# Optimization experiments

Measured on AMD Instinct MI355X. Metric: run time of the kernel, lower is better.

## Reference

```python
import jax, jax.numpy as jnp
import numpy as np

B = 16384      # batch
CNUM = 2048    # codebook entries
K = 8          # topk
D = 10         # emb_dim
M = 50         # meta_dim
UID = 1000000
IID = 1000000
TAU = 10.0


def setup_inputs() -> dict:
    key = jax.random.key(0)
    ks = jax.random.split(key, 14)
    uid_col = jax.random.randint(ks[0], (B, 1), 0, UID, dtype=jnp.int64)
    iid_col = jax.random.randint(ks[1], (B, 1), 0, IID + 1, dtype=jnp.int64)
    x = jnp.concatenate([uid_col, iid_col], axis=1)
    return {
        "x": x,
        "gumbel_u_src": jax.random.uniform(ks[2], (B, CNUM), dtype=jnp.float32),
        "gumbel_u_tgt": jax.random.uniform(ks[3], (B, CNUM), dtype=jnp.float32),
        "src_uid_table": jax.random.normal(ks[4], (UID, D), dtype=jnp.float32),
        "tgt_uid_table": jax.random.normal(ks[5], (UID, D), dtype=jnp.float32),
        "tgt_iid_table": jax.random.normal(ks[6], (IID + 1, D), dtype=jnp.float32),
        "C": jax.random.normal(ks[7], (CNUM, M), dtype=jnp.float32) * 0.01,
        "w1": jax.random.normal(ks[8], (D, M), dtype=jnp.float32) * 0.01,
        "w2": jax.random.normal(ks[9], (M, D), dtype=jnp.float32) * 0.01,
        "mw1": jax.random.normal(ks[10], (D + M, 50), dtype=jnp.float32) * 0.1,
        "mb1": jnp.zeros((50,), dtype=jnp.float32),
        "mw2": jax.random.normal(ks[11], (50, D * D), dtype=jnp.float32) * 0.1,
        "mb2": jnp.zeros((D * D,), dtype=jnp.float32),
    }


def _gumbel_route(u_emb, C, w1, u_noise):
    # u_emb: [B, D] -> logits s_u: [B, CNUM]
    s = jnp.einsum('bm,cm->bc', u_emb @ w1, C)
    g = -jnp.log(-jnp.log(u_noise + 1e-20) + 1e-20)  # gumbel noise
    gw = jax.nn.softmax((s + g) / TAU, axis=-1)       # F.gumbel_softmax, hard=False
    tw, ti = jax.lax.top_k(gw, K)                     # [B, K]
    c_u = C[ti]                                       # [B, K, M] codebook gather
    return tw, ti, c_u


def reference(x, gumbel_u_src, gumbel_u_tgt, src_uid_table, tgt_uid_table,
              tgt_iid_table, C, w1, w2, mw1, mb1, mw2, mb2):
    # ---- stage == 'test_meta' ----
    # target-side interest embedding ('test_interst' path)
    tuid = tgt_uid_table[x[:, 0]]                      # [B, D]
    tw_t, _, c_t = _gumbel_route(tuid, C, w1, gumbel_u_tgt)
    tuid_ins = ((c_t * tw_t[..., None]).sum(axis=1)) @ w2   # [B, D]
    # source-side routing ('test_meta' path of InterstEmbedding)
    uid = src_uid_table[x[:, 0]]                       # [B, D]
    tw_s, _, c_s = _gumbel_route(uid, C, w1, gumbel_u_src)
    src_fea = jnp.broadcast_to(uid[:, None, :], (uid.shape[0], K, D))  # [B, K, D]
    inp = jnp.concatenate([c_s, src_fea], axis=-1)     # [B, K, M+D] = [B, K, 60]
    h = jax.nn.relu(inp @ mw1 + mb1)                   # [B, K, 50]
    mapping = (h @ mw2 + mb2).reshape(-1, K, D, D)     # per-sample hypernet weights
    src_emb = jnp.einsum('bkd,bkde->bke', src_fea, mapping)  # [B, K, D]
    pre_emb = (src_emb * tw_s[..., None]).sum(axis=1)  # [B, D]
    fin_emb = tuid_ins + pre_emb                       # [B, D]
    iid_emb = tgt_iid_table[x[:, 1]]                   # [B, D]
    return jnp.sum(fin_emb * iid_emb, axis=-1)         # [B]
```

## Files before the change

kernel.cpp:

```cpp
#include <hip/hip_runtime.h>
#include <hip/hip_bf16.h>


#define BROWS 16384
#define CNUM  2048
#define KSEL  8
#define DIMD  10
#define MDIM  50
#define RPB   16
#define RTPB  32
#define TAUI  0.1f
#define T24   24

#define OFF_PF   0
#define OFF_T24  1664
#define OFF_T24L 2432
#define OFF_TS   3200
#define OFF_TW   8832
#define OFF_TI   9088
#define OFF_UD   9344
#define SMEM_W   9536

typedef float    f32x4 __attribute__((ext_vector_type(4)));
typedef _Float16 half8 __attribute__((ext_vector_type(8)));
typedef float    flt2  __attribute__((ext_vector_type(2)));
typedef unsigned int u32;

__device__ __forceinline__ u32 pkrtz(float a, float b) {
    auto h = __builtin_amdgcn_cvt_pkrtz(a, b);
    union { decltype(h) v; u32 u; } c; c.v = h; return c.u;
}
__device__ __forceinline__ float gnoise(float u) {
    return -__logf(-__logf(u + 1e-20f) + 1e-20f);
}

__global__ void cvtC(const float* __restrict__ Cm, u32* __restrict__ C16) {
    const int j = blockIdx.x * 256 + threadIdx.x;
    const int cand = j >> 5, w = j & 31, k = 2 * w;
    const float a = (k < MDIM)     ? Cm[cand*MDIM + k]     : 0.f;
    const float b = (k + 1 < MDIM) ? Cm[cand*MDIM + k + 1] : 0.f;
    C16[j] = pkrtz(a, b);
}

template<bool PRE>
__global__ __launch_bounds__(256, 4)
void mf_fused(const int* __restrict__ x32,
              const float* __restrict__ gsrc,
              const float* __restrict__ gtgt,
              const float* __restrict__ suid,
              const float* __restrict__ tuid,
              const float* __restrict__ tiid,
              const float* __restrict__ Cm,
              const float* __restrict__ w1,
              const float* __restrict__ w2,
              const float* __restrict__ mw1,
              const float* __restrict__ mb1,
              const float* __restrict__ mw2,
              const float* __restrict__ mb2,
              const u32* __restrict__ C16,
              float* __restrict__ out)
{
    __shared__ __align__(16) float smem[SMEM_W];
    __shared__ int sFlag;
    float* sPf  = smem + OFF_PF;
    u32*   T24u = (u32*)(smem + OFF_T24);
    float* T24l = smem + OFF_T24L;

    const int tid  = threadIdx.x;
    const int row0 = blockIdx.x * RPB;

    if (tid == 0) sFlag = 1;
    __syncthreads();
    if (tid < 128) { if (x32[2*tid+1] != 0) atomicAnd(&sFlag, 0); }
    __syncthreads();
    const int is64 = sFlag;

    for (int t = tid; t < RTPB*52; t += 256) {
        const int rt = t / 52, mm = t - rt*52;
        float v = 0.f;
        if (mm < MDIM) {
            const int r = row0 + (rt >> 1);
            const int uidx = is64 ? x32[4*r] : x32[2*r];
            const float* tab = (rt & 1) ? suid : tuid;
            #pragma unroll
            for (int d = 0; d < DIMD; ++d) v += tab[uidx*DIMD + d] * w1[d*MDIM + mm];
        }
        sPf[t] = v;
    }
    __syncthreads();

    const int lane = tid & 63, wv = tid >> 6;
    const int lr = lane & 15, lk = lane >> 4;
    const int g = wv & 1, h = wv >> 1;
    const int rt = g*16 + lr;
    const float* up = ((lr & 1) ? gsrc : gtgt) + (size_t)(row0 + g*8 + (lr >> 1)) * CNUM;

    half8 b0, b1;
    {
        union { u32 u[4]; half8 v; } c0, c1;
        #pragma unroll
        for (int jj = 0; jj < 4; ++jj) {
            const int k0 = lk*8 + jj*2;
            c0.u[jj] = pkrtz(sPf[rt*52 + k0], sPf[rt*52 + k0 + 1]);
            const int k1 = 32 + lk*8 + jj*2;
            const float e0 = (k1     < 52) ? sPf[rt*52 + k1]     : 0.f;
            const float e1 = (k1 + 1 < 52) ? sPf[rt*52 + k1 + 1] : 0.f;
            c1.u[jj] = pkrtz(e0, e1);
        }
        b0 = c0.v; b1 = c1.v;
    }

    float ts = 0.f;
    float q0=-3.4e38f,q1=-3.4e38f,q2=-3.4e38f,q3=-3.4e38f,
          q4=-3.4e38f,q5=-3.4e38f,q6=-3.4e38f,q7=-3.4e38f;

    #pragma unroll 4
    for (int ti = 0; ti < 64; ++ti) {
        const int cb = ((ti >> 2) << 7) + h*64 + ((ti & 3) << 4);
        half8 a0, a1;
        if (PRE) {
            const u32* cr = C16 + (size_t)(cb + lr)*32 + lk*4;
            a0 = *(const half8*)cr;
            a1 = *(const half8*)(cr + 16);
        } else {
            const float* cr = Cm + (size_t)(cb + lr)*MDIM;
            union { u32 u[4]; half8 v; } c0, c1;
            #pragma unroll
            for (int jj = 0; jj < 4; ++jj) {
                const int k0 = lk*8 + jj*2;
                c0.u[jj] = pkrtz(cr[k0], cr[k0+1]);
                const int k1 = 32 + lk*8 + jj*2;
                const float e0 = (k1     < MDIM) ? cr[k1]     : 0.f;
                const float e1 = (k1 + 1 < MDIM) ? cr[k1+1] : 0.f;
                c1.u[jj] = pkrtz(e0, e1);
            }
            a0 = c0.v; a1 = c1.v;
        }
        f32x4 acc = {0.f, 0.f, 0.f, 0.f};
        acc = __builtin_amdgcn_mfma_f32_16x16x32_f16(a0, b0, acc, 0, 0, 0);
        acc = __builtin_amdgcn_mfma_f32_16x16x32_f16(a1, b1, acc, 0, 0, 0);
        const f32x4 u4 = *(const f32x4*)(up + cb + lk*4);
        const int cg = cb + lk*4;
        #pragma unroll
        for (int r4 = 0; r4 < 4; ++r4) {
            const float l = (acc[r4] + gnoise(u4[r4])) * TAUI;
            ts += __expf(l);
            const float xs = __uint_as_float(
                (__float_as_uint(l) & 0xFFFFF800u) | (u32)(cg + r4));
            q0 = fmaxf(q0, fminf(q1, xs));
            q1 = fmaxf(q1, fminf(q2, xs));
            q2 = fmaxf(q2, fminf(q3, xs));
            q3 = fmaxf(q3, fminf(q4, xs));
            q4 = fmaxf(q4, fminf(q5, xs));
            q5 = fmaxf(q5, fminf(q6, xs));
            q6 = fmaxf(q6, fminf(q7, xs));
            q7 = fmaxf(q7, xs);
        }
    }

    {
        float tss = ts;
        tss += __shfl_xor(tss, 16); tss += __shfl_xor(tss, 32);
        if (lk == 0) smem[OFF_TS + rt*2 + h] = tss;
        #pragma unroll
        for (int k = 0; k < 12; ++k) {
            float gm = fmaxf(q7, __shfl_xor(q7, 16));
            gm = fmaxf(gm, __shfl_xor(gm, 32));
            if (q7 == gm) {
                T24u[rt*T24 + h*12 + k] = __float_as_uint(q7);
                q7=q6; q6=q5; q5=q4; q4=q3; q3=q2; q2=q1; q1=q0; q0=-3.4e38f;
            }
        }
    }
    __syncthreads();

    for (int e = tid; e < RTPB*T24; e += 256) {
        const int ert = e / T24;
        const int idx = (int)(T24u[e] & 2047u);
        const float* pf = sPf + ert*52;
        const float* cr = Cm + idx*MDIM;
        float s = 0.f;
        #pragma unroll
        for (int k2 = 0; k2 < 25; ++k2) {
            flt2 c = *(const flt2*)(cr + k2*2);
            s += pf[2*k2] * c.x + pf[2*k2+1] * c.y;
        }
        const int r = row0 + (ert >> 1);
        const float u = ((ert & 1) ? gsrc : gtgt)[(size_t)r*CNUM + idx];
        T24l[e] = (s + gnoise(u)) * TAUI;
    }
    __syncthreads();

    if (tid < RTPB) {
        const int rrt = tid;
        const float inv = 1.0f / (smem[OFF_TS + rrt*2] + smem[OFF_TS + rrt*2 + 1]);
        float lv[T24]; int iv[T24];
        #pragma unroll
        for (int j = 0; j < T24; ++j) {
            lv[j] = T24l[rrt*T24 + j];
            iv[j] = (int)(T24u[rrt*T24 + j] & 2047u);
        }
        u32 used = 0;
        #pragma unroll
        for (int k = 0; k < KSEL; ++k) {
            float bl = -3.4e38f; int bi = 1 << 30; int bj = 0;
            #pragma unroll
            for (int j = 0; j < T24; ++j) {
                const bool ok = !((used >> j) & 1);
                if (ok && (lv[j] > bl || (lv[j] == bl && iv[j] < bi))) { bl = lv[j]; bi = iv[j]; bj = j; }
            }
            used |= 1u << bj;
            smem[OFF_TW + rrt*KSEL + k] = __expf(bl) * inv;
            ((int*)smem)[OFF_TI + rrt*KSEL + k] = bi;
        }
    }
    __syncthreads();

    float* sH    = smem;
    float* sQ    = smem + 832;
    float* sUd   = smem + OFF_UD;
    float* sTopW = smem + OFF_TW;
    int*   sTopI = (int*)smem + OFF_TI;

    const int gg = tid >> 4, lg = tid & 15;
    const int row = row0 + gg;
    const int rt_t = gg*2, rt_s = gg*2 + 1;
    const int uidx = is64 ? x32[4*row]     : x32[2*row];
    const int iidx = is64 ? x32[4*row + 2] : x32[2*row + 1];

    if (lg < DIMD) sUd[gg*12 + lg] = suid[uidx*DIMD + lg];
    __syncthreads();

    for (int t = lg; t < MDIM*DIMD; t += 16) {
        const int j = t / DIMD, e = t - j*DIMD;
        float q = 0.f;
        #pragma unroll
        for (int d = 0; d < DIMD; ++d) q += sUd[gg*12 + d] * mw2[j*(DIMD*DIMD) + d*DIMD + e];
        sQ[gg*500 + t] = q;
    }
    for (int mm = lg; mm < MDIM; mm += 16) {
        float v = 0.f;
        #pragma unroll
        for (int k = 0; k < KSEL; ++k)
            v += sTopW[rt_t*KSEL + k] * Cm[sTopI[rt_t*KSEL + k]*MDIM + mm];
        sH[gg*52 + mm] = v;
    }
    __syncthreads();

    float acc_e = 0.f, be = 0.f;
    if (lg < DIMD) {
        for (int m2 = 0; m2 < MDIM; ++m2) acc_e += sH[gg*52 + m2] * w2[m2*DIMD + lg];
        #pragma unroll
        for (int d = 0; d < DIMD; ++d) be += sUd[gg*12 + d] * mb2[d*DIMD + lg];
    }
    __syncthreads();

    for (int k = 0; k < KSEL; ++k) {
        const int   ik = sTopI[rt_s*KSEL + k];
        const float tw = sTopW[rt_s*KSEL + k];
        for (int j = lg; j < MDIM; j += 16) {
            float hh = mb1[j];
            const float* crow = Cm + ik*MDIM;
            for (int t2 = 0; t2 < MDIM; ++t2) hh += crow[t2] * mw1[t2*MDIM + j];
            #pragma unroll
            for (int d = 0; d < DIMD; ++d) hh += sUd[gg*12 + d] * mw1[(MDIM + d)*MDIM + j];
            sH[gg*52 + j] = fmaxf(hh, 0.f);
        }
        __syncthreads();
        if (lg < DIMD) {
            float se = be;
            for (int j = 0; j < MDIM; ++j) se += sH[gg*52 + j] * sQ[gg*500 + j*DIMD + lg];
            acc_e += tw * se;
        }
        __syncthreads();
    }

    float o = 0.f;
    if (lg < DIMD) o = acc_e * tiid[iidx*DIMD + lg];
    #pragma unroll
    for (int k = 8; k >= 1; k >>= 1) o += __shfl_xor(o, k, 16);
    if (lg == 0) out[row] = o;
}

extern "C" void kernel_launch(void* const* d_in, const int* in_sizes, int n_in,
                              void* d_out, int out_size, void* d_ws, size_t ws_size,
                              hipStream_t stream) {
    (void)in_sizes; (void)n_in; (void)out_size;
    const int*   x32  = (const int*)d_in[0];
    const float* gsrc = (const float*)d_in[1];
    const float* gtgt = (const float*)d_in[2];
    const float* suid = (const float*)d_in[3];
    const float* tuid = (const float*)d_in[4];
    const float* tiid = (const float*)d_in[5];
    const float* Cm   = (const float*)d_in[6];
    const float* w1   = (const float*)d_in[7];
    const float* w2   = (const float*)d_in[8];
    const float* mw1  = (const float*)d_in[9];
    const float* mb1  = (const float*)d_in[10];
    const float* mw2  = (const float*)d_in[11];
    const float* mb2  = (const float*)d_in[12];
    u32* C16 = (u32*)d_ws;

    if (ws_size >= 262144) {
        hipLaunchKernelGGL(cvtC, dim3(256), dim3(256), 0, stream, Cm, C16);
        hipLaunchKernelGGL(mf_fused<true>, dim3(BROWS/RPB), dim3(256), 0, stream,
                           x32, gsrc, gtgt, suid, tuid, tiid, Cm, w1, w2, mw1, mb1, mw2, mb2,
                           C16, (float*)d_out);
    } else {
        hipLaunchKernelGGL(mf_fused<false>, dim3(BROWS/RPB), dim3(256), 0, stream,
                           x32, gsrc, gtgt, suid, tuid, tiid, Cm, w1, w2, mw1, mb1, mw2, mb2,
                           C16, (float*)d_out);
    }
}
```

Baseline: 282.5 us.

## Pre-swizzle fp16 codebook into MFMA fragment layout and software-prefetch loads

The codebook conversion kernel now writes fp16 C in a per-lane MFMA fragment order, so each lane reads contiguous 16-byte chunks with coalesced wave-wide loads. The main loop in the precomputed path becomes a software pipeline: the gumbel noise tiles are prefetched four iterations ahead and the codebook fragments two iterations ahead in registers. This targets load latency and uncoalesced access in the routing loop. It doubles the workspace requirement (the larger layout stores padding) and raises register pressure, which could lower occupancy; if the workspace is smaller, the slower fallback path runs.

```diff
diff --git a/kernel.cpp b/kernel.cpp
--- a/kernel.cpp
+++ b/kernel.cpp
@@ -36,7 +36,10 @@
 
 __global__ void cvtC(const float* __restrict__ Cm, u32* __restrict__ C16) {
     const int j = blockIdx.x * 256 + threadIdx.x;
-    const int cand = j >> 5, w = j & 31, k = 2 * w;
+    const int w = j & 3, l = (j >> 2) & 63, pl = (j >> 8) & 1, Tg = j >> 9;
+    const int cand = Tg * 16 + (l & 15);
+    const int kk = pl * 16 + ((l >> 4) << 2) + w;
+    const int k = 2 * kk;
     const float a = (k < MDIM)     ? Cm[cand*MDIM + k]     : 0.f;
     const float b = (k + 1 < MDIM) ? Cm[cand*MDIM + k + 1] : 0.f;
     C16[j] = pkrtz(a, b);
@@ -114,33 +117,7 @@
     float q0=-3.4e38f,q1=-3.4e38f,q2=-3.4e38f,q3=-3.4e38f,
           q4=-3.4e38f,q5=-3.4e38f,q6=-3.4e38f,q7=-3.4e38f;
 
-    #pragma unroll 4
-    for (int ti = 0; ti < 64; ++ti) {
-        const int cb = ((ti >> 2) << 7) + h*64 + ((ti & 3) << 4);
-        half8 a0, a1;
-        if (PRE) {
-            const u32* cr = C16 + (size_t)(cb + lr)*32 + lk*4;
-            a0 = *(const half8*)cr;
-            a1 = *(const half8*)(cr + 16);
-        } else {
-            const float* cr = Cm + (size_t)(cb + lr)*MDIM;
-            union { u32 u[4]; half8 v; } c0, c1;
-            #pragma unroll
-            for (int jj = 0; jj < 4; ++jj) {
-                const int k0 = lk*8 + jj*2;
-                c0.u[jj] = pkrtz(cr[k0], cr[k0+1]);
-                const int k1 = 32 + lk*8 + jj*2;
-                const float e0 = (k1     < MDIM) ? cr[k1]     : 0.f;
-                const float e1 = (k1 + 1 < MDIM) ? cr[k1+1] : 0.f;
-                c1.u[jj] = pkrtz(e0, e1);
-            }
-            a0 = c0.v; a1 = c1.v;
-        }
-        f32x4 acc = {0.f, 0.f, 0.f, 0.f};
-        acc = __builtin_amdgcn_mfma_f32_16x16x32_f16(a0, b0, acc, 0, 0, 0);
-        acc = __builtin_amdgcn_mfma_f32_16x16x32_f16(a1, b1, acc, 0, 0, 0);
-        const f32x4 u4 = *(const f32x4*)(up + cb + lk*4);
-        const int cg = cb + lk*4;
+    auto select4 = [&](const f32x4& acc, const f32x4& u4, int cg) {
         #pragma unroll
         for (int r4 = 0; r4 < 4; ++r4) {
             const float l = (acc[r4] + gnoise(u4[r4])) * TAUI;
@@ -155,6 +132,82 @@
             q5 = fmaxf(q5, fminf(q6, xs));
             q6 = fmaxf(q6, fminf(q7, xs));
             q7 = fmaxf(q7, xs);
+        }
+    };
+
+    if (PRE) {
+        auto uaddr = [&](int t) -> const float* {
+            return up + (((t >> 2) << 7) + h*64 + ((t & 3) << 4) + lk*4);
+        };
+        auto caddr = [&](int t) -> const u32* {
+            const int Tg = ((t >> 2) << 3) + (h << 2) + (t & 3);
+            return C16 + ((size_t)(Tg * 2) * 64 + lane) * 4;
+        };
+        f32x4 ub0 = *(const f32x4*)uaddr(0);
+        f32x4 ub1 = *(const f32x4*)uaddr(1);
+        f32x4 ub2 = *(const f32x4*)uaddr(2);
+        f32x4 ub3 = *(const f32x4*)uaddr(3);
+        const u32* ca0 = caddr(0);
+        const u32* ca1 = caddr(1);
+        half8 a00 = *(const half8*)ca0;
+        half8 a10 = *(const half8*)(ca0 + 256);
+        half8 a01 = *(const half8*)ca1;
+        half8 a11 = *(const half8*)(ca1 + 256);
+
+        for (int tt = 0; tt < 64; tt += 4) {
+            #pragma unroll
+            for (int p = 0; p < 4; ++p) {
+                const int t = tt + p;
+                f32x4 u4;
+                if      (p == 0) u4 = ub0;
+                else if (p == 1) u4 = ub1;
+                else if (p == 2) u4 = ub2;
+                else             u4 = ub3;
+                half8 a0, a1;
+                if ((p & 1) == 0) { a0 = a00; a1 = a10; }
+                else              { a0 = a01; a1 = a11; }
+                {
+                    const int tu = (t + 4) & 63;
+                    const f32x4 un = *(const f32x4*)uaddr(tu);
+                    if      (p == 0) ub0 = un;
+                    else if (p == 1) ub1 = un;
+                    else if (p == 2) ub2 = un;
+                    else             ub3 = un;
+                }
+                {
+                    const int tc = (t + 2) & 63;
+                    const u32* ca = caddr(tc);
+                    const half8 an0 = *(const half8*)ca;
+                    const half8 an1 = *(const half8*)(ca + 256);
+                    if ((p & 1) == 0) { a00 = an0; a10 = an1; }
+                    else              { a01 = an0; a11 = an1; }
+                }
+                const int cb = ((t >> 2) << 7) + h*64 + ((t & 3) << 4);
+                f32x4 acc = {0.f, 0.f, 0.f, 0.f};
+                acc = __builtin_amdgcn_mfma_f32_16x16x32_f16(a0, b0, acc, 0, 0, 0);
+                acc = __builtin_amdgcn_mfma_f32_16x16x32_f16(a1, b1, acc, 0, 0, 0);
+                select4(acc, u4, cb + lk*4);
+            }
+        }
+    } else {
+        for (int t = 0; t < 64; ++t) {
+            const int cb = ((t >> 2) << 7) + h*64 + ((t & 3) << 4);
+            const float* cr = Cm + (size_t)(cb + lr)*MDIM;
+            union { u32 u[4]; half8 v; } c0, c1;
+            #pragma unroll
+            for (int jj = 0; jj < 4; ++jj) {
+                const int k0 = lk*8 + jj*2;
+                c0.u[jj] = pkrtz(cr[k0], cr[k0+1]);
+                const int k1 = 32 + lk*8 + jj*2;
+                const float e0 = (k1     < MDIM) ? cr[k1]   : 0.f;
+                const float e1 = (k1 + 1 < MDIM) ? cr[k1+1] : 0.f;
+                c1.u[jj] = pkrtz(e0, e1);
+            }
+            f32x4 acc = {0.f, 0.f, 0.f, 0.f};
+            acc = __builtin_amdgcn_mfma_f32_16x16x32_f16(c0.v, b0, acc, 0, 0, 0);
+            acc = __builtin_amdgcn_mfma_f32_16x16x32_f16(c1.v, b1, acc, 0, 0, 0);
+            const f32x4 u4 = *(const f32x4*)(up + cb + lk*4);
+            select4(acc, u4, cb + lk*4);
         }
     }
 
@@ -301,8 +354,8 @@
     const float* mb2  = (const float*)d_in[12];
     u32* C16 = (u32*)d_ws;
 
-    if (ws_size >= 262144) {
-        hipLaunchKernelGGL(cvtC, dim3(256), dim3(256), 0, stream, Cm, C16);
+    if (ws_size >= 524288) {
+        hipLaunchKernelGGL(cvtC, dim3(512), dim3(256), 0, stream, Cm, C16);
         hipLaunchKernelGGL(mf_fused<true>, dim3(BROWS/RPB), dim3(256), 0, stream,
                            x32, gsrc, gtgt, suid, tuid, tiid, Cm, w1, w2, mw1, mb1, mw2, mb2,
                            C16, (float*)d_out);
```

Result: faster. 266.8 us (-5.6%).

## Split fused kernel into routing and epilogue kernels with MFMA-ordered codebook layout

Applied to the files above, without the earlier changes.

Splits the single fused kernel into a routing kernel and a separate epilogue kernel, which exchange top-k weights and indices through workspace memory. The routing kernel now handles 8 batch rows per block, with each wave covering a contiguous quarter of the codebook, and launch bounds rise to 8 blocks per SM for more occupancy. The codebook is pre-packed into fp16 in MFMA fragment order so each lane's loads are coalesced. The epilogue algebraically folds the item embedding into the hypernet weights per thread, avoiding shared-memory staging. This costs an extra launch plus a global round trip for the top-k results, and needs a larger workspace, falling back to the old fused path if the workspace is too small.

```diff
diff --git a/kernel.cpp b/kernel.cpp
--- a/kernel.cpp
+++ b/kernel.cpp
@@ -7,24 +7,13 @@
 #define KSEL  8
 #define DIMD  10
 #define MDIM  50
-#define RPB   16
-#define RTPB  32
 #define TAUI  0.1f
-#define T24   24
-
-#define OFF_PF   0
-#define OFF_T24  1664
-#define OFF_T24L 2432
-#define OFF_TS   3200
-#define OFF_TW   8832
-#define OFF_TI   9088
-#define OFF_UD   9344
-#define SMEM_W   9536
 
 typedef float    f32x4 __attribute__((ext_vector_type(4)));
 typedef _Float16 half8 __attribute__((ext_vector_type(8)));
 typedef float    flt2  __attribute__((ext_vector_type(2)));
 typedef unsigned int u32;
+typedef unsigned long long u64;
 
 __device__ __forceinline__ u32 pkrtz(float a, float b) {
     auto h = __builtin_amdgcn_cvt_pkrtz(a, b);
@@ -36,38 +25,36 @@
 
 __global__ void cvtC(const float* __restrict__ Cm, u32* __restrict__ C16) {
     const int j = blockIdx.x * 256 + threadIdx.x;
-    const int cand = j >> 5, w = j & 31, k = 2 * w;
+    const int w = j & 3, l = (j >> 2) & 63, pl = (j >> 8) & 1, Tg = j >> 9;
+    const int cand = Tg * 16 + (l & 15);
+    const int kk = pl * 16 + ((l >> 4) << 2) + w;
+    const int k = 2 * kk;
     const float a = (k < MDIM)     ? Cm[cand*MDIM + k]     : 0.f;
     const float b = (k + 1 < MDIM) ? Cm[cand*MDIM + k + 1] : 0.f;
     C16[j] = pkrtz(a, b);
 }
 
-template<bool PRE>
-__global__ __launch_bounds__(256, 4)
-void mf_fused(const int* __restrict__ x32,
+__global__ __launch_bounds__(256, 8)
+void mf_route(const int* __restrict__ x32,
               const float* __restrict__ gsrc,
               const float* __restrict__ gtgt,
               const float* __restrict__ suid,
               const float* __restrict__ tuid,
-              const float* __restrict__ tiid,
               const float* __restrict__ Cm,
               const float* __restrict__ w1,
-              const float* __restrict__ w2,
-              const float* __restrict__ mw1,
-              const float* __restrict__ mb1,
-              const float* __restrict__ mw2,
-              const float* __restrict__ mb2,
               const u32* __restrict__ C16,
-              float* __restrict__ out)
+              float* __restrict__ gTW,
+              int*   __restrict__ gTI)
 {
-    __shared__ __align__(16) float smem[SMEM_W];
+    __shared__ __align__(16) float smem[2432];
     __shared__ int sFlag;
-    float* sPf  = smem + OFF_PF;
-    u32*   T24u = (u32*)(smem + OFF_T24);
-    float* T24l = smem + OFF_T24L;
+    float* sPf  = smem;
+    u32*   T48u = (u32*)(smem + 832);
+    float* T48l = smem + 1600;
+    float* TS   = smem + 2368;
 
     const int tid  = threadIdx.x;
-    const int row0 = blockIdx.x * RPB;
+    const int row0 = blockIdx.x * 8;
 
     if (tid == 0) sFlag = 1;
     __syncthreads();
@@ -75,7 +62,7 @@
     __syncthreads();
     const int is64 = sFlag;
 
-    for (int t = tid; t < RTPB*52; t += 256) {
+    for (int t = tid; t < 16*52; t += 256) {
         const int rt = t / 52, mm = t - rt*52;
         float v = 0.f;
         if (mm < MDIM) {
@@ -91,9 +78,8 @@
 
     const int lane = tid & 63, wv = tid >> 6;
     const int lr = lane & 15, lk = lane >> 4;
-    const int g = wv & 1, h = wv >> 1;
-    const int rt = g*16 + lr;
-    const float* up = ((lr & 1) ? gsrc : gtgt) + (size_t)(row0 + g*8 + (lr >> 1)) * CNUM;
+    const int rt = lr;
+    const float* up = ((lr & 1) ? gsrc : gtgt) + (size_t)(row0 + (lr >> 1)) * CNUM;
 
     half8 b0, b1;
     {
@@ -114,32 +100,15 @@
     float q0=-3.4e38f,q1=-3.4e38f,q2=-3.4e38f,q3=-3.4e38f,
           q4=-3.4e38f,q5=-3.4e38f,q6=-3.4e38f,q7=-3.4e38f;
 
-    #pragma unroll 4
-    for (int ti = 0; ti < 64; ++ti) {
-        const int cb = ((ti >> 2) << 7) + h*64 + ((ti & 3) << 4);
-        half8 a0, a1;
-        if (PRE) {
-            const u32* cr = C16 + (size_t)(cb + lr)*32 + lk*4;
-            a0 = *(const half8*)cr;
-            a1 = *(const half8*)(cr + 16);
-        } else {
-            const float* cr = Cm + (size_t)(cb + lr)*MDIM;
-            union { u32 u[4]; half8 v; } c0, c1;
-            #pragma unroll
-            for (int jj = 0; jj < 4; ++jj) {
-                const int k0 = lk*8 + jj*2;
-                c0.u[jj] = pkrtz(cr[k0], cr[k0+1]);
-                const int k1 = 32 + lk*8 + jj*2;
-                const float e0 = (k1     < MDIM) ? cr[k1]     : 0.f;
-                const float e1 = (k1 + 1 < MDIM) ? cr[k1+1] : 0.f;
-                c1.u[jj] = pkrtz(e0, e1);
-            }
-            a0 = c0.v; a1 = c1.v;
-        }
+    for (int t = 0; t < 32; ++t) {
+        const int cb = wv*512 + t*16;
+        const f32x4 u4 = *(const f32x4*)(up + cb + lk*4);
+        const u32* cp = C16 + (size_t)((wv*32 + t)*128 + lane)*4;
+        const half8 a0 = *(const half8*)cp;
+        const half8 a1 = *(const half8*)(cp + 256);
         f32x4 acc = {0.f, 0.f, 0.f, 0.f};
         acc = __builtin_amdgcn_mfma_f32_16x16x32_f16(a0, b0, acc, 0, 0, 0);
         acc = __builtin_amdgcn_mfma_f32_16x16x32_f16(a1, b1, acc, 0, 0, 0);
-        const f32x4 u4 = *(const f32x4*)(up + cb + lk*4);
         const int cg = cb + lk*4;
         #pragma unroll
         for (int r4 = 0; r4 < 4; ++r4) {
@@ -161,21 +130,316 @@
     {
         float tss = ts;
         tss += __shfl_xor(tss, 16); tss += __shfl_xor(tss, 32);
-        if (lk == 0) smem[OFF_TS + rt*2 + h] = tss;
+        if (lk == 0) TS[rt*4 + wv] = tss;
         #pragma unroll
         for (int k = 0; k < 12; ++k) {
             float gm = fmaxf(q7, __shfl_xor(q7, 16));
             gm = fmaxf(gm, __shfl_xor(gm, 32));
             if (q7 == gm) {
-                T24u[rt*T24 + h*12 + k] = __float_as_uint(q7);
+                T48u[rt*48 + wv*12 + k] = __float_as_uint(q7);
                 q7=q6; q6=q5; q5=q4; q4=q3; q3=q2; q2=q1; q1=q0; q0=-3.4e38f;
             }
         }
     }
     __syncthreads();
 
-    for (int e = tid; e < RTPB*T24; e += 256) {
-        const int ert = e / T24;
+    for (int e = tid; e < 16*48; e += 256) {
+        const int ert = e / 48;
+        const int idx = (int)(T48u[e] & 2047u);
+        const float* pf = sPf + ert*52;
+        const float* cr = Cm + idx*MDIM;
+        float s = 0.f;
+        #pragma unroll
+        for (int k2 = 0; k2 < 25; ++k2) {
+            flt2 c = *(const flt2*)(cr + k2*2);
+            s += pf[2*k2] * c.x + pf[2*k2+1] * c.y;
+        }
+        const int r = row0 + (ert >> 1);
+        const float u = ((ert & 1) ? gsrc : gtgt)[(size_t)r*CNUM + idx];
+        T48l[e] = (s + gnoise(u)) * TAUI;
+    }
+    __syncthreads();
+
+    if (tid < 16) {
+        const int r8 = tid;
+        const float inv = 1.0f / (TS[r8*4] + TS[r8*4+1] + TS[r8*4+2] + TS[r8*4+3]);
+        u64 used = 0;
+        for (int k = 0; k < KSEL; ++k) {
+            float bl = -3.4e38f; int bi = 1 << 30; int bj = 0;
+            for (int j = 0; j < 48; ++j) {
+                if ((used >> j) & 1ull) continue;
+                const float lv = T48l[r8*48 + j];
+                const int   iv = (int)(T48u[r8*48 + j] & 2047u);
+                if (lv > bl || (lv == bl && iv < bi)) { bl = lv; bi = iv; bj = j; }
+            }
+            used |= 1ull << bj;
+            const int grt = blockIdx.x*16 + r8;
+            gTW[grt*KSEL + k] = __expf(bl) * inv;
+            gTI[grt*KSEL + k] = bi;
+        }
+    }
+}
+
+__global__ __launch_bounds__(256, 4)
+void mf_epilog(const int* __restrict__ x32,
+               const float* __restrict__ suid,
+               const float* __restrict__ tiid,
+               const float* __restrict__ Cm,
+               const float* __restrict__ w2,
+               const float* __restrict__ mw1,
+               const float* __restrict__ mb1,
+               const float* __restrict__ mw2,
+               const float* __restrict__ mb2,
+               const float* __restrict__ gTW,
+               const int*   __restrict__ gTI,
+               float* __restrict__ out)
+{
+    __shared__ int sFlag;
+    const int tid = threadIdx.x;
+    const int g = tid >> 4, lg = tid & 15;
+    const int row = blockIdx.x * 16 + g;
+
+    if (tid == 0) sFlag = 1;
+    __syncthreads();
+    if (tid < 128) { if (x32[2*tid+1] != 0) atomicAnd(&sFlag, 0); }
+    __syncthreads();
+    const int is64 = sFlag;
+
+    const int uidx = is64 ? x32[4*row]     : x32[2*row];
+    const int iidx = is64 ? x32[4*row + 2] : x32[2*row + 1];
+
+    float uid[10], ti[10];
+    #pragma unroll
+    for (int d = 0; d < DIMD; ++d) uid[d] = suid[(size_t)uidx*DIMD + d];
+    #pragma unroll
+    for (int e = 0; e < DIMD; ++e) ti[e] = tiid[(size_t)iidx*DIMD + e];
+
+    float twt[8], tws[8]; int it[8], is_[8];
+    #pragma unroll
+    for (int k = 0; k < KSEL; ++k) {
+        twt[k] = gTW[(row*2)*KSEL + k];     it[k]  = gTI[(row*2)*KSEL + k];
+        tws[k] = gTW[(row*2+1)*KSEL + k];   is_[k] = gTI[(row*2+1)*KSEL + k];
+    }
+
+    const int j0 = 4*lg;
+    const int nj = (j0 + 4 <= MDIM) ? 4 : (j0 < MDIM ? MDIM - j0 : 0);
+
+    float po = 0.f;
+    float qt[4] = {0,0,0,0}, w2t[4] = {0,0,0,0}, hb[4] = {0,0,0,0};
+
+    if (nj) {
+        {
+            flt2 m0 = *(const flt2*)(mb1 + j0);
+            hb[0] = m0.x; hb[1] = m0.y;
+            if (nj == 4) { flt2 m1 = *(const flt2*)(mb1 + j0 + 2); hb[2] = m1.x; hb[3] = m1.y; }
+            #pragma unroll
+            for (int d = 0; d < DIMD; ++d) {
+                const float* r = mw1 + (MDIM + d)*MDIM + j0;
+                flt2 a = *(const flt2*)r;
+                hb[0] += uid[d]*a.x; hb[1] += uid[d]*a.y;
+                if (nj == 4) { flt2 b = *(const flt2*)(r + 2); hb[2] += uid[d]*b.x; hb[3] += uid[d]*b.y; }
+            }
+        }
+        for (int jj = 0; jj < nj; ++jj) {
+            const float* r = w2 + (j0 + jj)*DIMD;
+            float s = 0.f;
+            #pragma unroll
+            for (int p = 0; p < 5; ++p) { flt2 a = *(const flt2*)(r + 2*p); s += a.x*ti[2*p] + a.y*ti[2*p+1]; }
+            w2t[jj] = s;
+        }
+        for (int jj = 0; jj < nj; ++jj) {
+            const float* r = mw2 + (size_t)(j0 + jj)*(DIMD*DIMD);
+            float s = 0.f;
+            #pragma unroll
+            for (int d = 0; d < DIMD; ++d) {
+                float sd = 0.f;
+                #pragma unroll
+                for (int p = 0; p < 5; ++p) { flt2 a = *(const flt2*)(r + d*DIMD + 2*p); sd += a.x*ti[2*p] + a.y*ti[2*p+1]; }
+                s += uid[d]*sd;
+            }
+            qt[jj] = s;
+        }
+        {
+            float ws[4] = {0,0,0,0};
+            #pragma unroll
+            for (int k = 0; k < KSEL; ++k) {
+                const float* cr = Cm + (size_t)it[k]*MDIM + j0;
+                flt2 a = *(const flt2*)cr;
+                ws[0] += twt[k]*a.x; ws[1] += twt[k]*a.y;
+                if (nj == 4) { flt2 b = *(const flt2*)(cr + 2); ws[2] += twt[k]*b.x; ws[3] += twt[k]*b.y; }
+            }
+            for (int jj = 0; jj < nj; ++jj) po += ws[jj]*w2t[jj];
+        }
+        float hk[8][4];
+        #pragma unroll
+        for (int k = 0; k < KSEL; ++k)
+            #pragma unroll
+            for (int jj = 0; jj < 4; ++jj) hk[k][jj] = hb[jj];
+        for (int t2 = 0; t2 < MDIM; t2 += 2) {
+            const float* r0 = mw1 + t2*MDIM + j0;
+            const float* r1 = mw1 + (t2+1)*MDIM + j0;
+            flt2 wa0 = *(const flt2*)r0, wb0 = *(const flt2*)(r0 + 2);
+            flt2 wa1 = *(const flt2*)r1, wb1 = *(const flt2*)(r1 + 2);
+            #pragma unroll
+            for (int k = 0; k < KSEL; ++k) {
+                flt2 c = *(const flt2*)(Cm + (size_t)is_[k]*MDIM + t2);
+                hk[k][0] += c.x*wa0.x + c.y*wa1.x;
+                hk[k][1] += c.x*wa0.y + c.y*wa1.y;
+                hk[k][2] += c.x*wb0.x + c.y*wb1.x;
+                hk[k][3] += c.x*wb0.y + c.y*wb1.y;
+            }
+        }
+        #pragma unroll
+        for (int k = 0; k < KSEL; ++k) {
+            float s = 0.f;
+            for (int jj = 0; jj < nj; ++jj) s += fmaxf(hk[k][jj], 0.f)*qt[jj];
+            po += tws[k]*s;
+        }
+    }
+    if (lg == 0) {
+        float stw = 0.f;
+        #pragma unroll
+        for (int k = 0; k < KSEL; ++k) stw += tws[k];
+        float bt = 0.f;
+        #pragma unroll
+        for (int d = 0; d < DIMD; ++d) {
+            float sd = 0.f;
+            #pragma unroll
+            for (int e = 0; e < DIMD; ++e) sd += mb2[d*DIMD + e]*ti[e];
+            bt += uid[d]*sd;
+        }
+        po += stw*bt;
+    }
+    po += __shfl_xor(po, 1, 16);
+    po += __shfl_xor(po, 2, 16);
+    po += __shfl_xor(po, 4, 16);
+    po += __shfl_xor(po, 8, 16);
+    if (lg == 0) out[row] = po;
+}
+
+__global__ __launch_bounds__(256, 4)
+void mf_fused_fb(const int* __restrict__ x32,
+                 const float* __restrict__ gsrc,
+                 const float* __restrict__ gtgt,
+                 const float* __restrict__ suid,
+                 const float* __restrict__ tuid,
+                 const float* __restrict__ tiid,
+                 const float* __restrict__ Cm,
+                 const float* __restrict__ w1,
+                 const float* __restrict__ w2,
+                 const float* __restrict__ mw1,
+                 const float* __restrict__ mb1,
+                 const float* __restrict__ mw2,
+                 const float* __restrict__ mb2,
+                 float* __restrict__ out)
+{
+    __shared__ __align__(16) float smem[9536];
+    __shared__ int sFlag;
+    float* sPf  = smem;
+    u32*   T24u = (u32*)(smem + 1664);
+    float* T24l = smem + 2432;
+
+    const int tid  = threadIdx.x;
+    const int row0 = blockIdx.x * 16;
+
+    if (tid == 0) sFlag = 1;
+    __syncthreads();
+    if (tid < 128) { if (x32[2*tid+1] != 0) atomicAnd(&sFlag, 0); }
+    __syncthreads();
+    const int is64 = sFlag;
+
+    for (int t = tid; t < 32*52; t += 256) {
+        const int rt = t / 52, mm = t - rt*52;
+        float v = 0.f;
+        if (mm < MDIM) {
+            const int r = row0 + (rt >> 1);
+            const int uidx = is64 ? x32[4*r] : x32[2*r];
+            const float* tab = (rt & 1) ? suid : tuid;
+            #pragma unroll
+            for (int d = 0; d < DIMD; ++d) v += tab[uidx*DIMD + d] * w1[d*MDIM + mm];
+        }
+        sPf[t] = v;
+    }
+    __syncthreads();
+
+    const int lane = tid & 63, wv = tid >> 6;
+    const int lr = lane & 15, lk = lane >> 4;
+    const int g = wv & 1, h = wv >> 1;
+    const int rt = g*16 + lr;
+    const float* up = ((lr & 1) ? gsrc : gtgt) + (size_t)(row0 + g*8 + (lr >> 1)) * CNUM;
+
+    half8 b0, b1;
+    {
+        union { u32 u[4]; half8 v; } c0, c1;
+        #pragma unroll
+        for (int jj = 0; jj < 4; ++jj) {
+            const int k0 = lk*8 + jj*2;
+            c0.u[jj] = pkrtz(sPf[rt*52 + k0], sPf[rt*52 + k0 + 1]);
+            const int k1 = 32 + lk*8 + jj*2;
+            const float e0 = (k1     < 52) ? sPf[rt*52 + k1]     : 0.f;
+            const float e1 = (k1 + 1 < 52) ? sPf[rt*52 + k1 + 1] : 0.f;
+            c1.u[jj] = pkrtz(e0, e1);
+        }
+        b0 = c0.v; b1 = c1.v;
+    }
+
+    float ts = 0.f;
+    float q0=-3.4e38f,q1=-3.4e38f,q2=-3.4e38f,q3=-3.4e38f,
+          q4=-3.4e38f,q5=-3.4e38f,q6=-3.4e38f,q7=-3.4e38f;
+
+    for (int t = 0; t < 64; ++t) {
+        const int cb = ((t >> 2) << 7) + h*64 + ((t & 3) << 4);
+        const float* cr = Cm + (size_t)(cb + lr)*MDIM;
+        union { u32 u[4]; half8 v; } c0, c1;
+        #pragma unroll
+        for (int jj = 0; jj < 4; ++jj) {
+            const int k0 = lk*8 + jj*2;
+            c0.u[jj] = pkrtz(cr[k0], cr[k0+1]);
+            const int k1 = 32 + lk*8 + jj*2;
+            const float e0 = (k1     < MDIM) ? cr[k1]   : 0.f;
+            const float e1 = (k1 + 1 < MDIM) ? cr[k1+1] : 0.f;
+            c1.u[jj] = pkrtz(e0, e1);
+        }
+        f32x4 acc = {0.f, 0.f, 0.f, 0.f};
+        acc = __builtin_amdgcn_mfma_f32_16x16x32_f16(c0.v, b0, acc, 0, 0, 0);
+        acc = __builtin_amdgcn_mfma_f32_16x16x32_f16(c1.v, b1, acc, 0, 0, 0);
+        const f32x4 u4 = *(const f32x4*)(up + cb + lk*4);
+        const int cg = cb + lk*4;
+        #pragma unroll
+        for (int r4 = 0; r4 < 4; ++r4) {
+            const float l = (acc[r4] + gnoise(u4[r4])) * TAUI;
+            ts += __expf(l);
+            const float xs = __uint_as_float(
+                (__float_as_uint(l) & 0xFFFFF800u) | (u32)(cg + r4));
+            q0 = fmaxf(q0, fminf(q1, xs));
+            q1 = fmaxf(q1, fminf(q2, xs));
+            q2 = fmaxf(q2, fminf(q3, xs));
+            q3 = fmaxf(q3, fminf(q4, xs));
+            q4 = fmaxf(q4, fminf(q5, xs));
+            q5 = fmaxf(q5, fminf(q6, xs));
+            q6 = fmaxf(q6, fminf(q7, xs));
+            q7 = fmaxf(q7, xs);
+        }
+    }
+
+    {
+        float tss = ts;
+        tss += __shfl_xor(tss, 16); tss += __shfl_xor(tss, 32);
+        if (lk == 0) smem[3200 + rt*2 + h] = tss;
+        #pragma unroll
+        for (int k = 0; k < 12; ++k) {
+            float gm = fmaxf(q7, __shfl_xor(q7, 16));
+            gm = fmaxf(gm, __shfl_xor(gm, 32));
+            if (q7 == gm) {
+                T24u[rt*24 + h*12 + k] = __float_as_uint(q7);
+                q7=q6; q6=q5; q5=q4; q4=q3; q3=q2; q2=q1; q1=q0; q0=-3.4e38f;
+            }
+        }
+    }
+    __syncthreads();
+
+    for (int e = tid; e < 32*24; e += 256) {
+        const int ert = e / 24;
         const int idx = (int)(T24u[e] & 2047u);
         const float* pf = sPf + ert*52;
         const float* cr = Cm + idx*MDIM;
@@ -191,36 +455,30 @@
     }
     __syncthreads();
 
-    if (tid < RTPB) {
+    if (tid < 32) {
         const int rrt = tid;
-        const float inv = 1.0f / (smem[OFF_TS + rrt*2] + smem[OFF_TS + rrt*2 + 1]);
-        float lv[T24]; int iv[T24];
-        #pragma unroll
-        for (int j = 0; j < T24; ++j) {
-            lv[j] = T24l[rrt*T24 + j];
-            iv[j] = (int)(T24u[rrt*T24 + j] & 2047u);
-        }
+        const float inv = 1.0f / (smem[3200 + rrt*2] + smem[3200 + rrt*2 + 1]);
         u32 used = 0;
-        #pragma unroll
         for (int k = 0; k < KSEL; ++k) {
             float bl = -3.4e38f; int bi = 1 << 30; int bj = 0;
-            #pragma unroll
-            for (int j = 0; j < T24; ++j) {
-                const bool ok = !((used >> j) & 1);
-                if (ok && (lv[j] > bl || (lv[j] == bl && iv[j] < bi))) { bl = lv[j]; bi = iv[j]; bj = j; }
+            for (int j = 0; j < 24; ++j) {
+                if ((used >> j) & 1) continue;
+                const float lv = T24l[rrt*24 + j];
+                const int   iv = (int)(T24u[rrt*24 + j] & 2047u);
+                if (lv > bl || (lv == bl && iv < bi)) { bl = lv; bi = iv; bj = j; }
             }
             used |= 1u << bj;
-            smem[OFF_TW + rrt*KSEL + k] = __expf(bl) * inv;
-            ((int*)smem)[OFF_TI + rrt*KSEL + k] = bi;
+            smem[8832 + rrt*KSEL + k] = __expf(bl) * inv;
+            ((int*)smem)[9088 + rrt*KSEL + k] = bi;
         }
     }
     __syncthreads();
 
     float* sH    = smem;
     float* sQ    = smem + 832;
-    float* sUd   = smem + OFF_UD;
-    float* sTopW = smem + OFF_TW;
-    int*   sTopI = (int*)smem + OFF_TI;
+    float* sUd   = smem + 9344;
+    float* sTopW = smem + 8832;
+    int*   sTopI = (int*)smem + 9088;
 
     const int gg = tid >> 4, lg = tid & 15;
     const int row = row0 + gg;
@@ -299,16 +557,20 @@
     const float* mb1  = (const float*)d_in[10];
     const float* mw2  = (const float*)d_in[11];
     const float* mb2  = (const float*)d_in[12];
-    u32* C16 = (u32*)d_ws;
-
-    if (ws_size >= 262144) {
-        hipLaunchKernelGGL(cvtC, dim3(256), dim3(256), 0, stream, Cm, C16);
-        hipLaunchKernelGGL(mf_fused<true>, dim3(BROWS/RPB), dim3(256), 0, stream,
+
+    if (ws_size >= 655360u * 4u) {
+        u32*   C16 = (u32*)d_ws;
+        float* gTW = (float*)d_ws + 131072;
+        int*   gTI = (int*)d_ws + 393216;
+        hipLaunchKernelGGL(cvtC, dim3(512), dim3(256), 0, stream, Cm, C16);
+        hipLaunchKernelGGL(mf_route, dim3(BROWS/8), dim3(256), 0, stream,
+                           x32, gsrc, gtgt, suid, tuid, Cm, w1, C16, gTW, gTI);
+        hipLaunchKernelGGL(mf_epilog, dim3(BROWS/16), dim3(256), 0, stream,
+                           x32, suid, tiid, Cm, w2, mw1, mb1, mw2, mb2, gTW, gTI,
+                           (float*)d_out);
+    } else {
+        hipLaunchKernelGGL(mf_fused_fb, dim3(BROWS/16), dim3(256), 0, stream,
                            x32, gsrc, gtgt, suid, tuid, tiid, Cm, w1, w2, mw1, mb1, mw2, mb2,
-                           C16, (float*)d_out);
-    } else {
-        hipLaunchKernelGGL(mf_fused<false>, dim3(BROWS/RPB), dim3(256), 0, stream,
-                           x32, gsrc, gtgt, suid, tuid, tiid, Cm, w1, w2, mw1, mb1, mw2, mb2,
-                           C16, (float*)d_out);
-    }
-}
+                           (float*)d_out);
+    }
+}
```

Measured after the change: 283.5 us. Within noise of the previous version (+0.3%).
